# Optimization experiments

Hardware: AMD Instinct MI355X
Metric: run time of the kernel (lower is better)

The kernel has to match this reference:

```python
import jax, jax.numpy as jnp
import numpy as np

B, Q, C, H, L, P, DFF, EXTRA = 4, 64, 384, 6, 5, 4, 1024, 128
SIZES = [(14, 14), (28, 28), (56, 56), (112, 112), (224, 224)]
S = sum(h * w for h, w in SIZES)
DH = C // H


def setup_inputs() -> dict:
    key = jax.random.key(0)
    ks = iter(jax.random.split(key, 64))
    rn = lambda shape, s=1.0: jax.random.normal(next(ks), shape, jnp.float32) * s
    inp = dict(
        tgt=rn((B, Q, C)),
        reference_points=jax.random.uniform(next(ks), (B, Q, 2), dtype=jnp.float32),
        src=rn((B, S, C)),
        extra_memory=rn((B, EXTRA, C)),
        src_valid_ratios=jnp.ones((B, L, 2), jnp.float32),
        src_spatial_shapes=jnp.asarray(SIZES, jnp.int32),
        src_level_start_index=jnp.asarray(np.cumsum([0] + [h * w for h, w in SIZES])[:-1], jnp.int32),
    )
    for name, shape in [("sa_in_w", (3 * C, C)), ("sa_out_w", (C, C)),
                        ("ea_in_w", (3 * C, C)), ("ea_out_w", (C, C)),
                        ("ms_off_w", (H * L * P * 2, C)), ("ms_attn_w", (H * L * P, C)),
                        ("ms_val_w", (C, C)), ("ms_out_w", (C, C)),
                        ("ffn_w1", (DFF, C)), ("ffn_w2", (C, DFF))]:
        inp[name] = rn(shape, 0.02)
    for name, n in [("sa_in_b", 3 * C), ("sa_out_b", C), ("ea_in_b", 3 * C), ("ea_out_b", C),
                    ("ms_attn_b", H * L * P), ("ms_val_b", C), ("ms_out_b", C),
                    ("ffn_b1", DFF), ("ffn_b2", C),
                    ("ln2_b", C), ("lne_b", C), ("ln1_b", C), ("ln3_b", C)]:
        inp[name] = jnp.zeros((n,), jnp.float32)
    inp["ms_off_b"] = rn((H * L * P * 2,), 0.5)  # nonzero so sampling is off-grid
    for name in ["ln2_g", "lne_g", "ln1_g", "ln3_g"]:
        inp[name] = jnp.ones((C,), jnp.float32)
    return inp


def layer_norm(x, g, b, eps=1e-5):
    mu = x.mean(-1, keepdims=True)
    var = ((x - mu) ** 2).mean(-1, keepdims=True)
    return (x - mu) / jnp.sqrt(var + eps) * g + b


def mha(q_in, k_in, v_in, in_w, in_b, out_w, out_b):
    d = q_in.shape[-1]
    wq, wk, wv = in_w[:d], in_w[d:2 * d], in_w[2 * d:]
    bq, bk, bv = in_b[:d], in_b[d:2 * d], in_b[2 * d:]
    proj = lambda x, w, bias: (x @ w.T + bias).reshape(x.shape[0], x.shape[1], H, DH)
    q = proj(q_in, wq, bq)
    k = proj(k_in, wk, bk)
    v = proj(v_in, wv, bv)
    scores = jnp.einsum('bqhd,bkhd->bhqk', q, k) * (1.0 / np.sqrt(DH))
    a = jax.nn.softmax(scores, axis=-1)
    o = jnp.einsum('bhqk,bkhd->bqhd', a, v).reshape(q_in.shape[0], q_in.shape[1], d)
    return o @ out_w.T + out_b


def bilinear_sample(img, x, y):
    # img [N,Hh,Ww,D]; x,y [N,M] in pixel coords; zeros padding (grid_sample align_corners=False)
    N, Hh, Ww, D = img.shape
    x0 = jnp.floor(x)
    y0 = jnp.floor(y)
    wx = (x - x0)[..., None]
    wy = (y - y0)[..., None]
    rows = jnp.arange(N)[:, None]

    def g(xi, yi):
        valid = (xi >= 0) & (xi <= Ww - 1) & (yi >= 0) & (yi <= Hh - 1)
        xc = jnp.clip(xi, 0, Ww - 1).astype(jnp.int32)
        yc = jnp.clip(yi, 0, Hh - 1).astype(jnp.int32)
        return img[rows, yc, xc] * valid[..., None]

    v00 = g(x0, y0)
    v01 = g(x0 + 1, y0)
    v10 = g(x0, y0 + 1)
    v11 = g(x0 + 1, y0 + 1)
    top = v00 * (1 - wx) + v01 * wx
    bot = v10 * (1 - wx) + v11 * wx
    return top * (1 - wy) + bot * wy


def ms_deform_attn(query, ref_pts, src, spatial, lsi,
                   off_w, off_b, aw_w, aw_b, val_w, val_b, out_w, out_b):
    # query [B,Q,C], ref_pts [B,Q,L,2] normalized
    value = (src @ val_w.T + val_b).reshape(B, S, H, DH)
    off = (query @ off_w.T + off_b).reshape(B, Q, H, L, P, 2)
    aw = jax.nn.softmax((query @ aw_w.T + aw_b).reshape(B, Q, H, L * P), -1).reshape(B, Q, H, L, P)
    normalizer = jnp.asarray([[w_, h_] for h_, w_ in spatial], jnp.float32)  # [L,2] (W,H)
    loc = ref_pts[:, :, None, :, None, :] + off / normalizer[None, None, None, :, None, :]
    out = jnp.zeros((B, Q, H, DH), jnp.float32)
    for l, (h_, w_) in enumerate(spatial):
        h_, w_ = int(h_), int(w_)
        s0 = int(lsi[l])
        v_l = value[:, s0:s0 + h_ * w_].transpose(0, 2, 1, 3).reshape(B * H, h_, w_, DH)
        xy = loc[:, :, :, l].transpose(0, 2, 1, 3, 4).reshape(B * H, Q * P, 2)
        x = xy[..., 0] * w_ - 0.5
        y = xy[..., 1] * h_ - 0.5
        samp = bilinear_sample(v_l, x, y).reshape(B, H, Q, P, DH)
        out = out + jnp.einsum('bhqpd,bqhp->bqhd', samp, aw[:, :, :, l])
    return out.reshape(B, Q, C) @ out_w.T + out_b


def reference(tgt, reference_points, src, extra_memory, src_valid_ratios,
              src_spatial_shapes, src_level_start_index,
              sa_in_w, sa_in_b, sa_out_w, sa_out_b,
              ea_in_w, ea_in_b, ea_out_w, ea_out_b,
              ms_off_w, ms_off_b, ms_attn_w, ms_attn_b,
              ms_val_w, ms_val_b, ms_out_w, ms_out_b,
              ffn_w1, ffn_b1, ffn_w2, ffn_b2,
              ln2_g, ln2_b, lne_g, lne_b, ln1_g, ln1_b, ln3_g, ln3_b):
    spatial = np.asarray(jax.device_get(src_spatial_shapes))
    lsi = np.asarray(jax.device_get(src_level_start_index))
    # reference_points_input = ref[:, :, None] * valid_ratios[:, None] -> [B,Q,L,2]
    rp_in = reference_points[:, :, None] * src_valid_ratios[:, None]
    # self attention (query_pos is None)
    t2 = mha(tgt, tgt, tgt, sa_in_w, sa_in_b, sa_out_w, sa_out_b)
    tgt = layer_norm(tgt + t2, ln2_g, ln2_b)
    # extra cross attention over concatenated first/previous memory
    t2 = mha(tgt, extra_memory, extra_memory, ea_in_w, ea_in_b, ea_out_w, ea_out_b)
    tgt = layer_norm(tgt + t2, lne_g, lne_b)
    # multi-scale deformable cross attention
    t2 = ms_deform_attn(tgt, rp_in, src, spatial, lsi,
                        ms_off_w, ms_off_b, ms_attn_w, ms_attn_b,
                        ms_val_w, ms_val_b, ms_out_w, ms_out_b)
    tgt = layer_norm(tgt + t2, ln1_g, ln1_b)
    # FFN
    t2 = jax.nn.relu(tgt @ ffn_w1.T + ffn_b1) @ ffn_w2.T + ffn_b2
    tgt = layer_norm(tgt + t2, ln3_g, ln3_b)
    return tgt
```

## Files before the change

### kernel.cpp

```cpp
#include <hip/hip_runtime.h>
#include <hip/hip_bf16.h>

#define B_ 4
#define Q_ 64
#define C_ 384
#define H_ 6
#define L_ 5
#define P_ 4
#define DFF_ 1024
#define EXTRA_ 128
#define DH_ 64
#define S_ 66836

__device__ __forceinline__ float wave_sum(float v) {
    for (int off = 32; off; off >>= 1) v += __shfl_xor(v, off);
    return v;
}
__device__ __forceinline__ float wave_max(float v) {
    for (int off = 32; off; off >>= 1) v = fmaxf(v, __shfl_xor(v, off));
    return v;
}
__device__ __forceinline__ float block_sum6(float v, float* red, int t) {
    v = wave_sum(v);
    if ((t & 63) == 0) red[t >> 6] = v;
    __syncthreads();
    float s = red[0] + red[1] + red[2] + red[3] + red[4] + red[5];
    __syncthreads();
    return s;
}

__global__ void linear4_kernel(const float* __restrict__ in, const float* __restrict__ W,
                               const float* __restrict__ bias, float* __restrict__ out,
                               int K, int OUT, int relu) {
    int j = blockIdx.x * blockDim.x + threadIdx.x;
    int r0 = blockIdx.y * 4;
    if (j >= OUT) return;
    const float* wp = W + (size_t)j * K;
    const float* i0 = in + (size_t)r0 * K;
    const float* i1 = i0 + K;
    const float* i2 = i1 + K;
    const float* i3 = i2 + K;
    float a0 = 0.f, a1 = 0.f, a2 = 0.f, a3 = 0.f;
#pragma unroll 4
    for (int k = 0; k < K; k += 4) {
        float4 w = *reinterpret_cast<const float4*>(wp + k);
        float4 x0 = *reinterpret_cast<const float4*>(i0 + k);
        float4 x1 = *reinterpret_cast<const float4*>(i1 + k);
        float4 x2 = *reinterpret_cast<const float4*>(i2 + k);
        float4 x3 = *reinterpret_cast<const float4*>(i3 + k);
        a0 += w.x * x0.x + w.y * x0.y + w.z * x0.z + w.w * x0.w;
        a1 += w.x * x1.x + w.y * x1.y + w.z * x1.z + w.w * x1.w;
        a2 += w.x * x2.x + w.y * x2.y + w.z * x2.z + w.w * x2.w;
        a3 += w.x * x3.x + w.y * x3.y + w.z * x3.z + w.w * x3.w;
    }
    float bb = bias[j];
    a0 += bb; a1 += bb; a2 += bb; a3 += bb;
    if (relu) { a0 = fmaxf(a0, 0.f); a1 = fmaxf(a1, 0.f); a2 = fmaxf(a2, 0.f); a3 = fmaxf(a3, 0.f); }
    out[(size_t)(r0 + 0) * OUT + j] = a0;
    out[(size_t)(r0 + 1) * OUT + j] = a1;
    out[(size_t)(r0 + 2) * OUT + j] = a2;
    out[(size_t)(r0 + 3) * OUT + j] = a3;
}

__global__ void sa_fused_kernel(const float* __restrict__ qkv, const float* __restrict__ res,
                                const float* __restrict__ Wo, const float* __restrict__ bo,
                                const float* __restrict__ g, const float* __restrict__ beta,
                                float* __restrict__ out) {
    int row = blockIdx.x;
    int b = row >> 6;
    int t = threadIdx.x;
    int h = t >> 6, lane = t & 63;
    __shared__ float q_lds[384], a_lds[384], o_lds[384], red[8];
    q_lds[t] = qkv[(size_t)row * 1152 + t];
    __syncthreads();
    const float* krow = qkv + (size_t)(b * 64 + lane) * 1152 + 384 + h * 64;
    float s = 0.f;
#pragma unroll 8
    for (int d = 0; d < 64; ++d) s += q_lds[h * 64 + d] * krow[d];
    s *= 0.125f;
    float m = wave_max(s);
    float e = __expf(s - m);
    float sum = wave_sum(e);
    a_lds[t] = e / sum;
    __syncthreads();
    float acc = 0.f;
#pragma unroll 4
    for (int k = 0; k < 64; ++k)
        acc += a_lds[h * 64 + k] * qkv[(size_t)(b * 64 + k) * 1152 + 768 + h * 64 + lane];
    o_lds[t] = acc;
    __syncthreads();
    const float* wp = Wo + (size_t)t * 384;
    float v = bo[t] + res[(size_t)row * 384 + t];
#pragma unroll 4
    for (int k = 0; k < 384; k += 4) {
        float4 w = *reinterpret_cast<const float4*>(wp + k);
        v += w.x * o_lds[k] + w.y * o_lds[k + 1] + w.z * o_lds[k + 2] + w.w * o_lds[k + 3];
    }
    float mean = block_sum6(v, red, t) * (1.f / 384.f);
    float d = v - mean;
    float var = block_sum6(d * d, red, t) * (1.f / 384.f);
    out[(size_t)row * 384 + t] = d * rsqrtf(var + 1e-5f) * g[t] + beta[t];
}

__global__ void ea_fused_kernel(const float* __restrict__ t1, const float* __restrict__ kv,
                                const float* __restrict__ Wq, const float* __restrict__ bq,
                                const float* __restrict__ Wo, const float* __restrict__ bo,
                                const float* __restrict__ g, const float* __restrict__ beta,
                                float* __restrict__ out) {
    int row = blockIdx.x;
    int b = row >> 6;
    int t = threadIdx.x;
    int h = t >> 6, lane = t & 63;
    __shared__ float in_lds[384], q_lds[384], a_lds[768], o_lds[384], red[8];
    in_lds[t] = t1[(size_t)row * 384 + t];
    __syncthreads();
    const float* wq = Wq + (size_t)t * 384;
    float qv = bq[t];
#pragma unroll 4
    for (int k = 0; k < 384; k += 4) {
        float4 w = *reinterpret_cast<const float4*>(wq + k);
        qv += w.x * in_lds[k] + w.y * in_lds[k + 1] + w.z * in_lds[k + 2] + w.w * in_lds[k + 3];
    }
    q_lds[t] = qv;
    __syncthreads();
    const float* k0 = kv + (size_t)(b * 128 + lane) * 768 + h * 64;
    const float* k1 = k0 + (size_t)64 * 768;
    float s0 = 0.f, s1 = 0.f;
#pragma unroll 8
    for (int d = 0; d < 64; ++d) { float qd = q_lds[h * 64 + d]; s0 += qd * k0[d]; s1 += qd * k1[d]; }
    s0 *= 0.125f; s1 *= 0.125f;
    float m = wave_max(fmaxf(s0, s1));
    float e0 = __expf(s0 - m), e1 = __expf(s1 - m);
    float sum = wave_sum(e0 + e1);
    a_lds[h * 128 + lane] = e0 / sum;
    a_lds[h * 128 + 64 + lane] = e1 / sum;
    __syncthreads();
    float acc = 0.f;
#pragma unroll 4
    for (int k = 0; k < 128; ++k)
        acc += a_lds[h * 128 + k] * kv[(size_t)(b * 128 + k) * 768 + 384 + h * 64 + lane];
    o_lds[t] = acc;
    __syncthreads();
    const float* wo = Wo + (size_t)t * 384;
    float v = bo[t] + in_lds[t];
#pragma unroll 4
    for (int k = 0; k < 384; k += 4) {
        float4 w = *reinterpret_cast<const float4*>(wo + k);
        v += w.x * o_lds[k] + w.y * o_lds[k + 1] + w.z * o_lds[k + 2] + w.w * o_lds[k + 3];
    }
    float mean = block_sum6(v, red, t) * (1.f / 384.f);
    float d = v - mean;
    float var = block_sum6(d * d, red, t) * (1.f / 384.f);
    out[(size_t)row * 384 + t] = d * rsqrtf(var + 1e-5f) * g[t] + beta[t];
}

__global__ void ms_prep_kernel(const float* __restrict__ t2, const float* __restrict__ Woff,
                               const float* __restrict__ boff, const float* __restrict__ Wa,
                               const float* __restrict__ ba, float* __restrict__ offs,
                               float* __restrict__ aw) {
    int row = blockIdx.x;
    int t = threadIdx.x;
    __shared__ float in_lds[384], lg[120];
    in_lds[t] = t2[(size_t)row * 384 + t];
    __syncthreads();
    if (t < 240) {
        const float* wp = Woff + (size_t)t * 384;
        float v = boff[t];
#pragma unroll 4
        for (int k = 0; k < 384; k += 4) {
            float4 w = *reinterpret_cast<const float4*>(wp + k);
            v += w.x * in_lds[k] + w.y * in_lds[k + 1] + w.z * in_lds[k + 2] + w.w * in_lds[k + 3];
        }
        offs[(size_t)row * 240 + t] = v;
    } else if (t < 360) {
        int j = t - 240;
        const float* wp = Wa + (size_t)j * 384;
        float v = ba[j];
#pragma unroll 4
        for (int k = 0; k < 384; k += 4) {
            float4 w = *reinterpret_cast<const float4*>(wp + k);
            v += w.x * in_lds[k] + w.y * in_lds[k + 1] + w.z * in_lds[k + 2] + w.w * in_lds[k + 3];
        }
        lg[j] = v;
    }
    __syncthreads();
    if (t < 6) {
        float m = -1e30f;
#pragma unroll
        for (int k = 0; k < 20; ++k) m = fmaxf(m, lg[t * 20 + k]);
        float e[20]; float s = 0.f;
#pragma unroll
        for (int k = 0; k < 20; ++k) { e[k] = __expf(lg[t * 20 + k] - m); s += e[k]; }
        float inv = 1.f / s;
#pragma unroll
        for (int k = 0; k < 20; ++k) aw[(size_t)row * 120 + t * 20 + k] = e[k] * inv;
    }
}

__global__ void ms_gather_kernel(const float* __restrict__ src, const float* __restrict__ refp,
                                 const float* __restrict__ vr, const float* __restrict__ offs,
                                 const float* __restrict__ aw, float* __restrict__ pagg,
                                 float* __restrict__ pwsum) {
    int l = blockIdx.x, h = blockIdx.y, row = blockIdx.z;
    int b = row >> 6;
    int t = threadIdx.x;
    const int lsi[5] = {0, 196, 980, 4116, 16660};
    const int whl[5] = {14, 28, 56, 112, 224};
    int wh = whl[l];
    float Wf = (float)wh;
    float rpx = refp[row * 2 + 0] * vr[(b * 5 + l) * 2 + 0];
    float rpy = refp[row * 2 + 1] * vr[(b * 5 + l) * 2 + 1];
    const float* srcb = src + ((size_t)b * S_ + lsi[l]) * 384;
    float acc0 = 0.f, acc1 = 0.f, acc2 = 0.f, wsm = 0.f;
#pragma unroll
    for (int p = 0; p < 4; ++p) {
        int oidx = row * 240 + ((h * 5 + l) * 4 + p) * 2;
        float ox = offs[oidx], oy = offs[oidx + 1];
        float locx = rpx + ox / Wf;
        float locy = rpy + oy / Wf;
        float x = locx * Wf - 0.5f;
        float y = locy * Wf - 0.5f;
        float x0 = floorf(x), y0 = floorf(y);
        float wx = x - x0, wy = y - y0;
        float a = aw[row * 120 + h * 20 + l * 4 + p];
        float cw[4] = {(1.f - wx) * (1.f - wy), wx * (1.f - wy), (1.f - wx) * wy, wx * wy};
        float cx[4] = {x0, x0 + 1.f, x0, x0 + 1.f};
        float cy[4] = {y0, y0, y0 + 1.f, y0 + 1.f};
#pragma unroll
        for (int c2 = 0; c2 < 4; ++c2) {
            bool valid = (cx[c2] >= 0.f) && (cx[c2] <= Wf - 1.f) &&
                         (cy[c2] >= 0.f) && (cy[c2] <= Wf - 1.f);
            if (!valid) continue;
            float w = a * cw[c2];
            wsm += w;
            int xi = (int)cx[c2], yi = (int)cy[c2];
            const float* sp = srcb + (size_t)(yi * wh + xi) * 384;
            acc0 += w * sp[t];
            acc1 += w * sp[t + 128];
            acc2 += w * sp[t + 256];
        }
    }
    float* ap = pagg + ((size_t)(row * 6 + h) * 5 + l) * 384;
    ap[t] = acc0; ap[t + 128] = acc1; ap[t + 256] = acc2;
    if (t == 0) pwsum[(row * 6 + h) * 5 + l] = wsm;
}

__global__ void ms_valout_kernel(const float* __restrict__ pagg, const float* __restrict__ pwsum,
                                 const float* __restrict__ Wv, const float* __restrict__ bv,
                                 const float* __restrict__ Wo, const float* __restrict__ bo,
                                 const float* __restrict__ t2, const float* __restrict__ g,
                                 const float* __restrict__ beta, float* __restrict__ out) {
    int row = blockIdx.x;
    int t = threadIdx.x;
    __shared__ float agg[2304], val[384], wsum[6], red[8];
#pragma unroll
    for (int e = 0; e < 6; ++e) {
        int idx = t + e * 384;
        int hh = idx / 384, col = idx % 384;
        const float* pp = pagg + ((size_t)(row * 6 + hh) * 5) * 384 + col;
        agg[idx] = pp[0] + pp[384] + pp[768] + pp[1152] + pp[1536];
    }
    if (t < 6) {
        const float* pw = pwsum + (row * 6 + t) * 5;
        wsum[t] = pw[0] + pw[1] + pw[2] + pw[3] + pw[4];
    }
    __syncthreads();
    int h = t >> 6;
    const float* wp = Wv + (size_t)t * 384;
    const float* ag = agg + h * 384;
    float v = bv[t] * wsum[h];
#pragma unroll 4
    for (int k = 0; k < 384; k += 4) {
        float4 w = *reinterpret_cast<const float4*>(wp + k);
        v += w.x * ag[k] + w.y * ag[k + 1] + w.z * ag[k + 2] + w.w * ag[k + 3];
    }
    val[t] = v;
    __syncthreads();
    const float* wo = Wo + (size_t)t * 384;
    float o = bo[t] + t2[(size_t)row * 384 + t];
#pragma unroll 4
    for (int k = 0; k < 384; k += 4) {
        float4 w = *reinterpret_cast<const float4*>(wo + k);
        o += w.x * val[k] + w.y * val[k + 1] + w.z * val[k + 2] + w.w * val[k + 3];
    }
    float mean = block_sum6(o, red, t) * (1.f / 384.f);
    float d = o - mean;
    float var = block_sum6(d * d, red, t) * (1.f / 384.f);
    out[(size_t)row * 384 + t] = d * rsqrtf(var + 1e-5f) * g[t] + beta[t];
}

__global__ void add_ln_kernel(const float* __restrict__ x, const float* __restrict__ r,
                              const float* __restrict__ g, const float* __restrict__ bgb,
                              float* __restrict__ out) {
    int row = blockIdx.x;
    int t = threadIdx.x;
    float v[6];
    float mean = 0.f;
#pragma unroll
    for (int i = 0; i < 6; ++i) {
        int c = t + i * 64;
        v[i] = x[(size_t)row * C_ + c] + r[(size_t)row * C_ + c];
        mean += v[i];
    }
    mean = wave_sum(mean) * (1.f / C_);
    float var = 0.f;
#pragma unroll
    for (int i = 0; i < 6; ++i) { float d = v[i] - mean; var += d * d; }
    var = wave_sum(var) * (1.f / C_);
    float inv = rsqrtf(var + 1e-5f);
#pragma unroll
    for (int i = 0; i < 6; ++i) {
        int c = t + i * 64;
        out[(size_t)row * C_ + c] = (v[i] - mean) * inv * g[c] + bgb[c];
    }
}

extern "C" void kernel_launch(void* const* d_in, const int* in_sizes, int n_in,
                              void* d_out, int out_size, void* d_ws, size_t ws_size,
                              hipStream_t stream) {
    const float* tgt   = (const float*)d_in[0];
    const float* refp  = (const float*)d_in[1];
    const float* src   = (const float*)d_in[2];
    const float* extra = (const float*)d_in[3];
    const float* vr    = (const float*)d_in[4];
    const float* sa_in_w  = (const float*)d_in[7];
    const float* sa_out_w = (const float*)d_in[8];
    const float* ea_in_w  = (const float*)d_in[9];
    const float* ea_out_w = (const float*)d_in[10];
    const float* ms_off_w = (const float*)d_in[11];
    const float* ms_attn_w= (const float*)d_in[12];
    const float* ms_val_w = (const float*)d_in[13];
    const float* ms_out_w = (const float*)d_in[14];
    const float* ffn_w1   = (const float*)d_in[15];
    const float* ffn_w2   = (const float*)d_in[16];
    const float* sa_in_b  = (const float*)d_in[17];
    const float* sa_out_b = (const float*)d_in[18];
    const float* ea_in_b  = (const float*)d_in[19];
    const float* ea_out_b = (const float*)d_in[20];
    const float* ms_attn_b= (const float*)d_in[21];
    const float* ms_val_b = (const float*)d_in[22];
    const float* ms_out_b = (const float*)d_in[23];
    const float* ffn_b1   = (const float*)d_in[24];
    const float* ffn_b2   = (const float*)d_in[25];
    const float* ln2_b    = (const float*)d_in[26];
    const float* lne_b    = (const float*)d_in[27];
    const float* ln1_b    = (const float*)d_in[28];
    const float* ln3_b    = (const float*)d_in[29];
    const float* ms_off_b = (const float*)d_in[30];
    const float* ln2_g    = (const float*)d_in[31];
    const float* lne_g    = (const float*)d_in[32];
    const float* ln1_g    = (const float*)d_in[33];
    const float* ln3_g    = (const float*)d_in[34];

    float* ws = (float*)d_ws;
    float* s_qkv  = ws;
    float* s_eakv = s_qkv + 294912;
    float* s_t1   = s_eakv + 393216;
    float* s_t2   = s_t1 + 98304;
    float* s_t3   = s_t2 + 98304;
    float* s_off  = s_t3 + 98304;
    float* s_aw   = s_off + 61440;
    float* s_pagg = s_aw + 30720;
    float* s_pws  = s_pagg + 2949120;
    float* s_h1   = s_pws + 7680;
    float* s_f2   = s_h1 + 262144;

    linear4_kernel<<<dim3(9, 64), dim3(128), 0, stream>>>(tgt, sa_in_w, sa_in_b, s_qkv, C_, 3 * C_, 0);
    linear4_kernel<<<dim3(6, 128), dim3(128), 0, stream>>>(extra, ea_in_w + (size_t)C_ * C_, ea_in_b + C_, s_eakv, C_, 2 * C_, 0);
    sa_fused_kernel<<<dim3(256), dim3(384), 0, stream>>>(s_qkv, tgt, sa_out_w, sa_out_b, ln2_g, ln2_b, s_t1);
    ea_fused_kernel<<<dim3(256), dim3(384), 0, stream>>>(s_t1, s_eakv, ea_in_w, ea_in_b, ea_out_w, ea_out_b, lne_g, lne_b, s_t2);
    ms_prep_kernel<<<dim3(256), dim3(384), 0, stream>>>(s_t2, ms_off_w, ms_off_b, ms_attn_w, ms_attn_b, s_off, s_aw);
    ms_gather_kernel<<<dim3(5, 6, 256), dim3(128), 0, stream>>>(src, refp, vr, s_off, s_aw, s_pagg, s_pws);
    ms_valout_kernel<<<dim3(256), dim3(384), 0, stream>>>(s_pagg, s_pws, ms_val_w, ms_val_b, ms_out_w, ms_out_b, s_t2, ln1_g, ln1_b, s_t3);
    linear4_kernel<<<dim3(8, 64), dim3(128), 0, stream>>>(s_t3, ffn_w1, ffn_b1, s_h1, C_, DFF_, 1);
    linear4_kernel<<<dim3(3, 64), dim3(128), 0, stream>>>(s_h1, ffn_w2, ffn_b2, s_f2, DFF_, C_, 0);
    add_ln_kernel<<<dim3(256), dim3(64), 0, stream>>>(s_f2, s_t3, ln3_g, ln3_b, (float*)d_out);
}
```

Before: 282.4 us.

## Split fused per-row kernels into LDS-tiled 16-row linears plus separate attention/LN

Replaces per-row fused attention+projection+layernorm kernels, where every block reread full weight matrices for one row, with a generic 16-row tiled linear kernel that stages inputs in LDS and reuses each weight load across 16 rows. Attention cores, layernorms, the offset/logit projection and the value projection become separate kernels. The attention-weight softmax moves into the gather kernel. Weight traffic drops a lot, but kernel launches grow from 10 to 17, grids shrink to roughly 96 blocks, and intermediates make extra global round trips.

```diff
diff --git a/kernel.cpp b/kernel.cpp
--- a/kernel.cpp
+++ b/kernel.cpp
@@ -12,6 +12,9 @@
 #define DH_ 64
 #define S_ 66836
 
+#define FLAG_RELU 1
+#define FLAG_RES 2
+
 __device__ __forceinline__ float wave_sum(float v) {
     for (int off = 32; off; off >>= 1) v += __shfl_xor(v, off);
     return v;
@@ -20,57 +23,98 @@
     for (int off = 32; off; off >>= 1) v = fmaxf(v, __shfl_xor(v, off));
     return v;
 }
-__device__ __forceinline__ float block_sum6(float v, float* red, int t) {
-    v = wave_sum(v);
-    if ((t & 63) == 0) red[t >> 6] = v;
-    __syncthreads();
-    float s = red[0] + red[1] + red[2] + red[3] + red[4] + red[5];
-    __syncthreads();
-    return s;
-}
-
-__global__ void linear4_kernel(const float* __restrict__ in, const float* __restrict__ W,
-                               const float* __restrict__ bias, float* __restrict__ out,
-                               int K, int OUT, int relu) {
-    int j = blockIdx.x * blockDim.x + threadIdx.x;
-    int r0 = blockIdx.y * 4;
+
+__global__ __launch_bounds__(256) void lin16_kernel(
+        const float* __restrict__ in, const float* __restrict__ W,
+        const float* __restrict__ bias, const float* __restrict__ res,
+        float* __restrict__ out, int K, int OUT, int flags) {
+    extern __shared__ float xs[];
+    int t = threadIdx.x;
+    int r0 = blockIdx.y * 16;
+    int K4 = K >> 2;
+    const float4* in4 = reinterpret_cast<const float4*>(in + (size_t)r0 * K);
+    float4* xs4 = reinterpret_cast<float4*>(xs);
+    for (int i = t; i < 16 * K4; i += 256) xs4[i] = in4[i];
+    __syncthreads();
+    int j = blockIdx.x * 64 + (t & 63);
+    int rg = t >> 6;
     if (j >= OUT) return;
-    const float* wp = W + (size_t)j * K;
-    const float* i0 = in + (size_t)r0 * K;
-    const float* i1 = i0 + K;
-    const float* i2 = i1 + K;
-    const float* i3 = i2 + K;
+    const float4* wp = reinterpret_cast<const float4*>(W + (size_t)j * K);
+    const float4* x0 = reinterpret_cast<const float4*>(xs + (rg * 4 + 0) * K);
+    const float4* x1 = reinterpret_cast<const float4*>(xs + (rg * 4 + 1) * K);
+    const float4* x2 = reinterpret_cast<const float4*>(xs + (rg * 4 + 2) * K);
+    const float4* x3 = reinterpret_cast<const float4*>(xs + (rg * 4 + 3) * K);
     float a0 = 0.f, a1 = 0.f, a2 = 0.f, a3 = 0.f;
 #pragma unroll 4
-    for (int k = 0; k < K; k += 4) {
-        float4 w = *reinterpret_cast<const float4*>(wp + k);
-        float4 x0 = *reinterpret_cast<const float4*>(i0 + k);
-        float4 x1 = *reinterpret_cast<const float4*>(i1 + k);
-        float4 x2 = *reinterpret_cast<const float4*>(i2 + k);
-        float4 x3 = *reinterpret_cast<const float4*>(i3 + k);
-        a0 += w.x * x0.x + w.y * x0.y + w.z * x0.z + w.w * x0.w;
-        a1 += w.x * x1.x + w.y * x1.y + w.z * x1.z + w.w * x1.w;
-        a2 += w.x * x2.x + w.y * x2.y + w.z * x2.z + w.w * x2.w;
-        a3 += w.x * x3.x + w.y * x3.y + w.z * x3.z + w.w * x3.w;
+    for (int k = 0; k < K4; ++k) {
+        float4 w = wp[k];
+        float4 v0 = x0[k], v1 = x1[k], v2 = x2[k], v3 = x3[k];
+        a0 += w.x * v0.x + w.y * v0.y + w.z * v0.z + w.w * v0.w;
+        a1 += w.x * v1.x + w.y * v1.y + w.z * v1.z + w.w * v1.w;
+        a2 += w.x * v2.x + w.y * v2.y + w.z * v2.z + w.w * v2.w;
+        a3 += w.x * v3.x + w.y * v3.y + w.z * v3.z + w.w * v3.w;
     }
     float bb = bias[j];
-    a0 += bb; a1 += bb; a2 += bb; a3 += bb;
-    if (relu) { a0 = fmaxf(a0, 0.f); a1 = fmaxf(a1, 0.f); a2 = fmaxf(a2, 0.f); a3 = fmaxf(a3, 0.f); }
-    out[(size_t)(r0 + 0) * OUT + j] = a0;
-    out[(size_t)(r0 + 1) * OUT + j] = a1;
-    out[(size_t)(r0 + 2) * OUT + j] = a2;
-    out[(size_t)(r0 + 3) * OUT + j] = a3;
-}
-
-__global__ void sa_fused_kernel(const float* __restrict__ qkv, const float* __restrict__ res,
-                                const float* __restrict__ Wo, const float* __restrict__ bo,
-                                const float* __restrict__ g, const float* __restrict__ beta,
-                                float* __restrict__ out) {
+    float v[4] = {a0 + bb, a1 + bb, a2 + bb, a3 + bb};
+    int orow = r0 + rg * 4;
+#pragma unroll
+    for (int i = 0; i < 4; ++i) {
+        float o = v[i];
+        if (flags & FLAG_RES) o += res[(size_t)(orow + i) * OUT + j];
+        if (flags & FLAG_RELU) o = fmaxf(o, 0.f);
+        out[(size_t)(orow + i) * OUT + j] = o;
+    }
+}
+
+__global__ __launch_bounds__(256) void prep_kernel(
+        const float* __restrict__ in, const float* __restrict__ Woff,
+        const float* __restrict__ boff, const float* __restrict__ Wa,
+        const float* __restrict__ ba, float* __restrict__ offs,
+        float* __restrict__ lg) {
+    extern __shared__ float xs[];
+    int t = threadIdx.x;
+    int r0 = blockIdx.y * 16;
+    const float4* in4 = reinterpret_cast<const float4*>(in + (size_t)r0 * 384);
+    float4* xs4 = reinterpret_cast<float4*>(xs);
+    for (int i = t; i < 16 * 96; i += 256) xs4[i] = in4[i];
+    __syncthreads();
+    int j = blockIdx.x * 64 + (t & 63);
+    int rg = t >> 6;
+    if (j >= 360) return;
+    const float4* wp;
+    float bb;
+    if (j < 240) { wp = reinterpret_cast<const float4*>(Woff + (size_t)j * 384); bb = boff[j]; }
+    else         { wp = reinterpret_cast<const float4*>(Wa + (size_t)(j - 240) * 384); bb = ba[j - 240]; }
+    const float4* x0 = reinterpret_cast<const float4*>(xs + (rg * 4 + 0) * 384);
+    const float4* x1 = reinterpret_cast<const float4*>(xs + (rg * 4 + 1) * 384);
+    const float4* x2 = reinterpret_cast<const float4*>(xs + (rg * 4 + 2) * 384);
+    const float4* x3 = reinterpret_cast<const float4*>(xs + (rg * 4 + 3) * 384);
+    float a0 = 0.f, a1 = 0.f, a2 = 0.f, a3 = 0.f;
+#pragma unroll 4
+    for (int k = 0; k < 96; ++k) {
+        float4 w = wp[k];
+        float4 v0 = x0[k], v1 = x1[k], v2 = x2[k], v3 = x3[k];
+        a0 += w.x * v0.x + w.y * v0.y + w.z * v0.z + w.w * v0.w;
+        a1 += w.x * v1.x + w.y * v1.y + w.z * v1.z + w.w * v1.w;
+        a2 += w.x * v2.x + w.y * v2.y + w.z * v2.z + w.w * v2.w;
+        a3 += w.x * v3.x + w.y * v3.y + w.z * v3.z + w.w * v3.w;
+    }
+    float v[4] = {a0 + bb, a1 + bb, a2 + bb, a3 + bb};
+    int orow = r0 + rg * 4;
+#pragma unroll
+    for (int i = 0; i < 4; ++i) {
+        if (j < 240) offs[(size_t)(orow + i) * 240 + j] = v[i];
+        else         lg[(size_t)(orow + i) * 120 + (j - 240)] = v[i];
+    }
+}
+
+__global__ __launch_bounds__(384) void sa_attn_kernel(const float* __restrict__ qkv,
+                                                      float* __restrict__ o) {
     int row = blockIdx.x;
     int b = row >> 6;
     int t = threadIdx.x;
     int h = t >> 6, lane = t & 63;
-    __shared__ float q_lds[384], a_lds[384], o_lds[384], red[8];
+    __shared__ float q_lds[384], a_lds[384];
     q_lds[t] = qkv[(size_t)row * 1152 + t];
     __syncthreads();
     const float* krow = qkv + (size_t)(b * 64 + lane) * 1152 + 384 + h * 64;
@@ -87,41 +131,18 @@
 #pragma unroll 4
     for (int k = 0; k < 64; ++k)
         acc += a_lds[h * 64 + k] * qkv[(size_t)(b * 64 + k) * 1152 + 768 + h * 64 + lane];
-    o_lds[t] = acc;
-    __syncthreads();
-    const float* wp = Wo + (size_t)t * 384;
-    float v = bo[t] + res[(size_t)row * 384 + t];
-#pragma unroll 4
-    for (int k = 0; k < 384; k += 4) {
-        float4 w = *reinterpret_cast<const float4*>(wp + k);
-        v += w.x * o_lds[k] + w.y * o_lds[k + 1] + w.z * o_lds[k + 2] + w.w * o_lds[k + 3];
-    }
-    float mean = block_sum6(v, red, t) * (1.f / 384.f);
-    float d = v - mean;
-    float var = block_sum6(d * d, red, t) * (1.f / 384.f);
-    out[(size_t)row * 384 + t] = d * rsqrtf(var + 1e-5f) * g[t] + beta[t];
-}
-
-__global__ void ea_fused_kernel(const float* __restrict__ t1, const float* __restrict__ kv,
-                                const float* __restrict__ Wq, const float* __restrict__ bq,
-                                const float* __restrict__ Wo, const float* __restrict__ bo,
-                                const float* __restrict__ g, const float* __restrict__ beta,
-                                float* __restrict__ out) {
+    o[(size_t)row * 384 + t] = acc;
+}
+
+__global__ __launch_bounds__(384) void ea_attn_kernel(const float* __restrict__ q,
+                                                      const float* __restrict__ kv,
+                                                      float* __restrict__ o) {
     int row = blockIdx.x;
     int b = row >> 6;
     int t = threadIdx.x;
     int h = t >> 6, lane = t & 63;
-    __shared__ float in_lds[384], q_lds[384], a_lds[768], o_lds[384], red[8];
-    in_lds[t] = t1[(size_t)row * 384 + t];
-    __syncthreads();
-    const float* wq = Wq + (size_t)t * 384;
-    float qv = bq[t];
-#pragma unroll 4
-    for (int k = 0; k < 384; k += 4) {
-        float4 w = *reinterpret_cast<const float4*>(wq + k);
-        qv += w.x * in_lds[k] + w.y * in_lds[k + 1] + w.z * in_lds[k + 2] + w.w * in_lds[k + 3];
-    }
-    q_lds[t] = qv;
+    __shared__ float q_lds[384], a_lds[768];
+    q_lds[t] = q[(size_t)row * 384 + t];
     __syncthreads();
     const float* k0 = kv + (size_t)(b * 128 + lane) * 768 + h * 64;
     const float* k1 = k0 + (size_t)64 * 768;
@@ -139,68 +160,40 @@
 #pragma unroll 4
     for (int k = 0; k < 128; ++k)
         acc += a_lds[h * 128 + k] * kv[(size_t)(b * 128 + k) * 768 + 384 + h * 64 + lane];
-    o_lds[t] = acc;
-    __syncthreads();
-    const float* wo = Wo + (size_t)t * 384;
-    float v = bo[t] + in_lds[t];
-#pragma unroll 4
-    for (int k = 0; k < 384; k += 4) {
-        float4 w = *reinterpret_cast<const float4*>(wo + k);
-        v += w.x * o_lds[k] + w.y * o_lds[k + 1] + w.z * o_lds[k + 2] + w.w * o_lds[k + 3];
-    }
-    float mean = block_sum6(v, red, t) * (1.f / 384.f);
-    float d = v - mean;
-    float var = block_sum6(d * d, red, t) * (1.f / 384.f);
-    out[(size_t)row * 384 + t] = d * rsqrtf(var + 1e-5f) * g[t] + beta[t];
-}
-
-__global__ void ms_prep_kernel(const float* __restrict__ t2, const float* __restrict__ Woff,
-                               const float* __restrict__ boff, const float* __restrict__ Wa,
-                               const float* __restrict__ ba, float* __restrict__ offs,
-                               float* __restrict__ aw) {
+    o[(size_t)row * 384 + t] = acc;
+}
+
+__global__ __launch_bounds__(64) void ln_kernel(const float* __restrict__ z,
+                                                const float* __restrict__ g,
+                                                const float* __restrict__ beta,
+                                                float* __restrict__ out) {
     int row = blockIdx.x;
     int t = threadIdx.x;
-    __shared__ float in_lds[384], lg[120];
-    in_lds[t] = t2[(size_t)row * 384 + t];
-    __syncthreads();
-    if (t < 240) {
-        const float* wp = Woff + (size_t)t * 384;
-        float v = boff[t];
-#pragma unroll 4
-        for (int k = 0; k < 384; k += 4) {
-            float4 w = *reinterpret_cast<const float4*>(wp + k);
-            v += w.x * in_lds[k] + w.y * in_lds[k + 1] + w.z * in_lds[k + 2] + w.w * in_lds[k + 3];
-        }
-        offs[(size_t)row * 240 + t] = v;
-    } else if (t < 360) {
-        int j = t - 240;
-        const float* wp = Wa + (size_t)j * 384;
-        float v = ba[j];
-#pragma unroll 4
-        for (int k = 0; k < 384; k += 4) {
-            float4 w = *reinterpret_cast<const float4*>(wp + k);
-            v += w.x * in_lds[k] + w.y * in_lds[k + 1] + w.z * in_lds[k + 2] + w.w * in_lds[k + 3];
-        }
-        lg[j] = v;
-    }
-    __syncthreads();
-    if (t < 6) {
-        float m = -1e30f;
-#pragma unroll
-        for (int k = 0; k < 20; ++k) m = fmaxf(m, lg[t * 20 + k]);
-        float e[20]; float s = 0.f;
-#pragma unroll
-        for (int k = 0; k < 20; ++k) { e[k] = __expf(lg[t * 20 + k] - m); s += e[k]; }
-        float inv = 1.f / s;
-#pragma unroll
-        for (int k = 0; k < 20; ++k) aw[(size_t)row * 120 + t * 20 + k] = e[k] * inv;
-    }
-}
-
-__global__ void ms_gather_kernel(const float* __restrict__ src, const float* __restrict__ refp,
-                                 const float* __restrict__ vr, const float* __restrict__ offs,
-                                 const float* __restrict__ aw, float* __restrict__ pagg,
-                                 float* __restrict__ pwsum) {
+    float v[6];
+    float mean = 0.f;
+#pragma unroll
+    for (int i = 0; i < 6; ++i) {
+        v[i] = z[(size_t)row * C_ + t + i * 64];
+        mean += v[i];
+    }
+    mean = wave_sum(mean) * (1.f / C_);
+    float var = 0.f;
+#pragma unroll
+    for (int i = 0; i < 6; ++i) { float d = v[i] - mean; var += d * d; }
+    var = wave_sum(var) * (1.f / C_);
+    float inv = rsqrtf(var + 1e-5f);
+#pragma unroll
+    for (int i = 0; i < 6; ++i) {
+        int c = t + i * 64;
+        out[(size_t)row * C_ + c] = (v[i] - mean) * inv * g[c] + beta[c];
+    }
+}
+
+__global__ __launch_bounds__(128) void ms_gather_kernel(
+        const float* __restrict__ src, const float* __restrict__ refp,
+        const float* __restrict__ vr, const float* __restrict__ offs,
+        const float* __restrict__ lg, float* __restrict__ pagg,
+        float* __restrict__ pwsum) {
     int l = blockIdx.x, h = blockIdx.y, row = blockIdx.z;
     int b = row >> 6;
     int t = threadIdx.x;
@@ -208,6 +201,14 @@
     const int whl[5] = {14, 28, 56, 112, 224};
     int wh = whl[l];
     float Wf = (float)wh;
+    const float* lp = lg + (size_t)row * 120 + h * 20;
+    float m = -1e30f;
+#pragma unroll
+    for (int k = 0; k < 20; ++k) m = fmaxf(m, lp[k]);
+    float denom = 0.f;
+#pragma unroll
+    for (int k = 0; k < 20; ++k) denom += __expf(lp[k] - m);
+    float dinv = 1.f / denom;
     float rpx = refp[row * 2 + 0] * vr[(b * 5 + l) * 2 + 0];
     float rpy = refp[row * 2 + 1] * vr[(b * 5 + l) * 2 + 1];
     const float* srcb = src + ((size_t)b * S_ + lsi[l]) * 384;
@@ -216,13 +217,11 @@
     for (int p = 0; p < 4; ++p) {
         int oidx = row * 240 + ((h * 5 + l) * 4 + p) * 2;
         float ox = offs[oidx], oy = offs[oidx + 1];
-        float locx = rpx + ox / Wf;
-        float locy = rpy + oy / Wf;
-        float x = locx * Wf - 0.5f;
-        float y = locy * Wf - 0.5f;
+        float x = (rpx + ox / Wf) * Wf - 0.5f;
+        float y = (rpy + oy / Wf) * Wf - 0.5f;
         float x0 = floorf(x), y0 = floorf(y);
         float wx = x - x0, wy = y - y0;
-        float a = aw[row * 120 + h * 20 + l * 4 + p];
+        float a = __expf(lp[l * 4 + p] - m) * dinv;
         float cw[4] = {(1.f - wx) * (1.f - wy), wx * (1.f - wy), (1.f - wx) * wy, wx * wy};
         float cx[4] = {x0, x0 + 1.f, x0, x0 + 1.f};
         float cy[4] = {y0, y0, y0 + 1.f, y0 + 1.f};
@@ -245,74 +244,56 @@
     if (t == 0) pwsum[(row * 6 + h) * 5 + l] = wsm;
 }
 
-__global__ void ms_valout_kernel(const float* __restrict__ pagg, const float* __restrict__ pwsum,
-                                 const float* __restrict__ Wv, const float* __restrict__ bv,
-                                 const float* __restrict__ Wo, const float* __restrict__ bo,
-                                 const float* __restrict__ t2, const float* __restrict__ g,
-                                 const float* __restrict__ beta, float* __restrict__ out) {
-    int row = blockIdx.x;
-    int t = threadIdx.x;
-    __shared__ float agg[2304], val[384], wsum[6], red[8];
-#pragma unroll
-    for (int e = 0; e < 6; ++e) {
-        int idx = t + e * 384;
-        int hh = idx / 384, col = idx % 384;
-        const float* pp = pagg + ((size_t)(row * 6 + hh) * 5) * 384 + col;
-        agg[idx] = pp[0] + pp[384] + pp[768] + pp[1152] + pp[1536];
-    }
-    if (t < 6) {
-        const float* pw = pwsum + (row * 6 + t) * 5;
-        wsum[t] = pw[0] + pw[1] + pw[2] + pw[3] + pw[4];
-    }
-    __syncthreads();
-    int h = t >> 6;
-    const float* wp = Wv + (size_t)t * 384;
-    const float* ag = agg + h * 384;
-    float v = bv[t] * wsum[h];
-#pragma unroll 4
-    for (int k = 0; k < 384; k += 4) {
-        float4 w = *reinterpret_cast<const float4*>(wp + k);
-        v += w.x * ag[k] + w.y * ag[k + 1] + w.z * ag[k + 2] + w.w * ag[k + 3];
-    }
-    val[t] = v;
-    __syncthreads();
-    const float* wo = Wo + (size_t)t * 384;
-    float o = bo[t] + t2[(size_t)row * 384 + t];
-#pragma unroll 4
-    for (int k = 0; k < 384; k += 4) {
-        float4 w = *reinterpret_cast<const float4*>(wo + k);
-        o += w.x * val[k] + w.y * val[k + 1] + w.z * val[k + 2] + w.w * val[k + 3];
-    }
-    float mean = block_sum6(o, red, t) * (1.f / 384.f);
-    float d = o - mean;
-    float var = block_sum6(d * d, red, t) * (1.f / 384.f);
-    out[(size_t)row * 384 + t] = d * rsqrtf(var + 1e-5f) * g[t] + beta[t];
-}
-
-__global__ void add_ln_kernel(const float* __restrict__ x, const float* __restrict__ r,
-                              const float* __restrict__ g, const float* __restrict__ bgb,
-                              float* __restrict__ out) {
-    int row = blockIdx.x;
-    int t = threadIdx.x;
-    float v[6];
-    float mean = 0.f;
-#pragma unroll
-    for (int i = 0; i < 6; ++i) {
-        int c = t + i * 64;
-        v[i] = x[(size_t)row * C_ + c] + r[(size_t)row * C_ + c];
-        mean += v[i];
-    }
-    mean = wave_sum(mean) * (1.f / C_);
-    float var = 0.f;
-#pragma unroll
-    for (int i = 0; i < 6; ++i) { float d = v[i] - mean; var += d * d; }
-    var = wave_sum(var) * (1.f / C_);
-    float inv = rsqrtf(var + 1e-5f);
-#pragma unroll
-    for (int i = 0; i < 6; ++i) {
-        int c = t + i * 64;
-        out[(size_t)row * C_ + c] = (v[i] - mean) * inv * g[c] + bgb[c];
-    }
+__global__ __launch_bounds__(256) void valproj_kernel(
+        const float* __restrict__ pagg, const float* __restrict__ pwsum,
+        const float* __restrict__ Wv, const float* __restrict__ bv,
+        float* __restrict__ val) {
+    __shared__ float xs[16 * 384];
+    __shared__ float ws16[16];
+    int t = threadIdx.x;
+    int h = blockIdx.x;
+    int r0 = blockIdx.y * 16;
+    float4* xs4 = reinterpret_cast<float4*>(xs);
+    for (int i = t; i < 16 * 96; i += 256) {
+        int row = i / 96, c4 = i % 96;
+        const float4* pp = reinterpret_cast<const float4*>(pagg) +
+                           ((size_t)((r0 + row) * 6 + h) * 5) * 96 + c4;
+        float4 s = pp[0];
+        float4 p1 = pp[96], p2 = pp[192], p3 = pp[288], p4 = pp[384];
+        s.x += p1.x + p2.x + p3.x + p4.x;
+        s.y += p1.y + p2.y + p3.y + p4.y;
+        s.z += p1.z + p2.z + p3.z + p4.z;
+        s.w += p1.w + p2.w + p3.w + p4.w;
+        xs4[i] = s;
+    }
+    if (t < 16) {
+        const float* pw = pwsum + ((size_t)(r0 + t) * 6 + h) * 5;
+        ws16[t] = pw[0] + pw[1] + pw[2] + pw[3] + pw[4];
+    }
+    __syncthreads();
+    int j = h * 64 + (t & 63);
+    int rg = t >> 6;
+    const float4* wp = reinterpret_cast<const float4*>(Wv + (size_t)j * 384);
+    const float4* x0 = reinterpret_cast<const float4*>(xs + (rg * 4 + 0) * 384);
+    const float4* x1 = reinterpret_cast<const float4*>(xs + (rg * 4 + 1) * 384);
+    const float4* x2 = reinterpret_cast<const float4*>(xs + (rg * 4 + 2) * 384);
+    const float4* x3 = reinterpret_cast<const float4*>(xs + (rg * 4 + 3) * 384);
+    float a0 = 0.f, a1 = 0.f, a2 = 0.f, a3 = 0.f;
+#pragma unroll 4
+    for (int k = 0; k < 96; ++k) {
+        float4 w = wp[k];
+        float4 v0 = x0[k], v1 = x1[k], v2 = x2[k], v3 = x3[k];
+        a0 += w.x * v0.x + w.y * v0.y + w.z * v0.z + w.w * v0.w;
+        a1 += w.x * v1.x + w.y * v1.y + w.z * v1.z + w.w * v1.w;
+        a2 += w.x * v2.x + w.y * v2.y + w.z * v2.z + w.w * v2.w;
+        a3 += w.x * v3.x + w.y * v3.y + w.z * v3.z + w.w * v3.w;
+    }
+    float bb = bv[j];
+    int orow = r0 + rg * 4;
+    float acc[4] = {a0, a1, a2, a3};
+#pragma unroll
+    for (int i = 0; i < 4; ++i)
+        val[(size_t)(orow + i) * 384 + j] = acc[i] + bb * ws16[rg * 4 + i];
 }
 
 extern "C" void kernel_launch(void* const* d_in, const int* in_sizes, int n_in,
@@ -354,25 +335,39 @@
 
     float* ws = (float*)d_ws;
     float* s_qkv  = ws;
-    float* s_eakv = s_qkv + 294912;
-    float* s_t1   = s_eakv + 393216;
-    float* s_t2   = s_t1 + 98304;
-    float* s_t3   = s_t2 + 98304;
-    float* s_off  = s_t3 + 98304;
-    float* s_aw   = s_off + 61440;
-    float* s_pagg = s_aw + 30720;
-    float* s_pws  = s_pagg + 2949120;
-    float* s_h1   = s_pws + 7680;
-    float* s_f2   = s_h1 + 262144;
-
-    linear4_kernel<<<dim3(9, 64), dim3(128), 0, stream>>>(tgt, sa_in_w, sa_in_b, s_qkv, C_, 3 * C_, 0);
-    linear4_kernel<<<dim3(6, 128), dim3(128), 0, stream>>>(extra, ea_in_w + (size_t)C_ * C_, ea_in_b + C_, s_eakv, C_, 2 * C_, 0);
-    sa_fused_kernel<<<dim3(256), dim3(384), 0, stream>>>(s_qkv, tgt, sa_out_w, sa_out_b, ln2_g, ln2_b, s_t1);
-    ea_fused_kernel<<<dim3(256), dim3(384), 0, stream>>>(s_t1, s_eakv, ea_in_w, ea_in_b, ea_out_w, ea_out_b, lne_g, lne_b, s_t2);
-    ms_prep_kernel<<<dim3(256), dim3(384), 0, stream>>>(s_t2, ms_off_w, ms_off_b, ms_attn_w, ms_attn_b, s_off, s_aw);
-    ms_gather_kernel<<<dim3(5, 6, 256), dim3(128), 0, stream>>>(src, refp, vr, s_off, s_aw, s_pagg, s_pws);
-    ms_valout_kernel<<<dim3(256), dim3(384), 0, stream>>>(s_pagg, s_pws, ms_val_w, ms_val_b, ms_out_w, ms_out_b, s_t2, ln1_g, ln1_b, s_t3);
-    linear4_kernel<<<dim3(8, 64), dim3(128), 0, stream>>>(s_t3, ffn_w1, ffn_b1, s_h1, C_, DFF_, 1);
-    linear4_kernel<<<dim3(3, 64), dim3(128), 0, stream>>>(s_h1, ffn_w2, ffn_b2, s_f2, DFF_, C_, 0);
-    add_ln_kernel<<<dim3(256), dim3(64), 0, stream>>>(s_f2, s_t3, ln3_g, ln3_b, (float*)d_out);
-}
+    float* s_eakv = ws + 294912;
+    float* s_osa  = ws + 688128;
+    float* s_z    = ws + 786432;
+    float* s_t1   = ws + 884736;
+    float* s_eaq  = ws + 983040;
+    float* s_oea  = ws + 1081344;
+    float* s_t2   = ws + 1179648;
+    float* s_off  = ws + 1277952;
+    float* s_lg   = ws + 1339392;
+    float* s_pagg = ws + 1370112;
+    float* s_pws  = ws + 4319232;
+    float* s_val  = ws + 4326912;
+    float* s_t3   = ws + 4425216;
+    float* s_h1   = ws + 4523520;
+
+    const size_t LDS384 = 16 * 384 * 4;
+    const size_t LDS1024 = 16 * 1024 * 4;
+
+    lin16_kernel<<<dim3(18, 16), 256, LDS384, stream>>>(tgt, sa_in_w, sa_in_b, nullptr, s_qkv, 384, 1152, 0);
+    lin16_kernel<<<dim3(12, 32), 256, LDS384, stream>>>(extra, ea_in_w + (size_t)C_ * C_, ea_in_b + C_, nullptr, s_eakv, 384, 768, 0);
+    sa_attn_kernel<<<dim3(256), dim3(384), 0, stream>>>(s_qkv, s_osa);
+    lin16_kernel<<<dim3(6, 16), 256, LDS384, stream>>>(s_osa, sa_out_w, sa_out_b, tgt, s_z, 384, 384, FLAG_RES);
+    ln_kernel<<<dim3(256), dim3(64), 0, stream>>>(s_z, ln2_g, ln2_b, s_t1);
+    lin16_kernel<<<dim3(6, 16), 256, LDS384, stream>>>(s_t1, ea_in_w, ea_in_b, nullptr, s_eaq, 384, 384, 0);
+    ea_attn_kernel<<<dim3(256), dim3(384), 0, stream>>>(s_eaq, s_eakv, s_oea);
+    lin16_kernel<<<dim3(6, 16), 256, LDS384, stream>>>(s_oea, ea_out_w, ea_out_b, s_t1, s_z, 384, 384, FLAG_RES);
+    ln_kernel<<<dim3(256), dim3(64), 0, stream>>>(s_z, lne_g, lne_b, s_t2);
+    prep_kernel<<<dim3(6, 16), 256, LDS384, stream>>>(s_t2, ms_off_w, ms_off_b, ms_attn_w, ms_attn_b, s_off, s_lg);
+    ms_gather_kernel<<<dim3(5, 6, 256), dim3(128), 0, stream>>>(src, refp, vr, s_off, s_lg, s_pagg, s_pws);
+    valproj_kernel<<<dim3(6, 16), 256, 0, stream>>>(s_pagg, s_pws, ms_val_w, ms_val_b, s_val);
+    lin16_kernel<<<dim3(6, 16), 256, LDS384, stream>>>(s_val, ms_out_w, ms_out_b, s_t2, s_z, 384, 384, FLAG_RES);
+    ln_kernel<<<dim3(256), dim3(64), 0, stream>>>(s_z, ln1_g, ln1_b, s_t3);
+    lin16_kernel<<<dim3(16, 16), 256, LDS384, stream>>>(s_t3, ffn_w1, ffn_b1, nullptr, s_h1, 384, 1024, FLAG_RELU);
+    lin16_kernel<<<dim3(6, 16), 256, LDS1024, stream>>>(s_h1, ffn_w2, ffn_b2, s_t3, s_z, 1024, 384, FLAG_RES);
+    ln_kernel<<<dim3(256), dim3(64), 0, stream>>>(s_z, ln3_g, ln3_b, (float*)d_out);
+}
```

New measurement: 296.5 us. 1.05x slower.
